# Kernel optimization log

Hardware: AMD Instinct MI355X
Metric: run time of the kernel (lower is better)

The kernel has to match this reference:

```python
import jax, jax.numpy as jnp
import numpy as np

B, N, DIN, H, A = 16384, 32, 275, 64, 14
NEG = 9000000000000000.0  # 9e15, matches torch source


def _att(x, mask, Wv, bv, Wk, bk, Wq, bq):
    # x: [B, N, H], mask: [B, N, N]
    v = jax.nn.relu(x @ Wv + bv)
    q = jax.nn.relu(x @ Wq + bq)
    k = jax.nn.relu(x @ Wk + bk)
    scores = jnp.einsum('bnh,bmh->bnm', q, k)
    att = jax.nn.softmax(scores * mask - NEG * (1.0 - mask), axis=2)
    return jnp.einsum('bnm,bmh->bnh', att, v)


def setup_inputs() -> dict:
    key = jax.random.key(0)
    ks = jax.random.split(key, 16)
    inputs = jax.random.normal(ks[0], (B * N, DIN), dtype=jnp.float32)
    hidden_state = jnp.zeros((B * N, H), dtype=jnp.float32)
    adj = jax.random.randint(ks[1], (B, N, N), 0, 2).astype(jnp.float32)
    eye = jnp.eye(N, dtype=jnp.float32)
    adj = jnp.maximum(adj, eye)  # agents always attend to themselves
    s = 1.0 / np.sqrt(DIN)
    sh = 1.0 / np.sqrt(H)
    p = {
        'W_enc': jax.random.uniform(ks[2], (DIN, H), minval=-s, maxval=s),
        'b_enc': jax.random.uniform(ks[3], (H,), minval=-s, maxval=s),
        'Wv1': jax.random.uniform(ks[4], (H, H), minval=-sh, maxval=sh),
        'bv1': jnp.zeros((H,), jnp.float32),
        'Wk1': jax.random.uniform(ks[5], (H, H), minval=-sh, maxval=sh),
        'bk1': jnp.zeros((H,), jnp.float32),
        'Wq1': jax.random.uniform(ks[6], (H, H), minval=-sh, maxval=sh),
        'bq1': jnp.zeros((H,), jnp.float32),
        'Wv2': jax.random.uniform(ks[7], (H, H), minval=-sh, maxval=sh),
        'bv2': jnp.zeros((H,), jnp.float32),
        'Wk2': jax.random.uniform(ks[8], (H, H), minval=-sh, maxval=sh),
        'bk2': jnp.zeros((H,), jnp.float32),
        'Wq2': jax.random.uniform(ks[9], (H, H), minval=-sh, maxval=sh),
        'bq2': jnp.zeros((H,), jnp.float32),
        'Wqn': jax.random.uniform(ks[10], (H, A), minval=-sh, maxval=sh),
        'bqn': jax.random.uniform(ks[11], (A,), minval=-sh, maxval=sh),
    }
    return dict(inputs=inputs, hidden_state=hidden_state, adj=adj, **p)


def reference(inputs, hidden_state, adj, W_enc, b_enc,
              Wv1, bv1, Wk1, bk1, Wq1, bq1,
              Wv2, bv2, Wk2, bk2, Wq2, bq2,
              Wqn, bqn):
    h1 = jax.nn.relu(inputs @ W_enc + b_enc)          # [B*N, H]
    h1 = h1.reshape(-1, N, H)                          # [B, N, H]
    h2 = _att(h1, adj, Wv1, bv1, Wk1, bk1, Wq1, bq1)   # [B, N, H]
    h3 = _att(h2, adj, Wv2, bv2, Wk2, bk2, Wq2, bq2)   # [B, N, H]
    q = h3 @ Wqn + bqn                                 # [B, N, A]
    return q, hidden_state
```

## Files before the change

### kernel.cpp

```cpp
#include <hip/hip_runtime.h>

#define NB 16384
#define NN 32
#define DK 275
#define HH 64
#define AA 14
#define Q_ELEMS   ((size_t)NB * NN * AA)
#define HID_ELEMS ((size_t)NB * NN * HH)

typedef unsigned short u16;
typedef unsigned int   u32;
typedef __attribute__((ext_vector_type(8))) short s8v;
typedef __attribute__((ext_vector_type(4))) float f4v;

#define MFMA(a,b,c) __builtin_amdgcn_mfma_f32_16x16x32_bf16((a),(b),(c),0,0,0)

__device__ __forceinline__ u16 bf_hi(float x){
    union{float f; u32 u;} v; v.f = x;
    u32 r = v.u + 0x7fffu + ((v.u >> 16) & 1u);
    return (u16)(r >> 16);
}
__device__ __forceinline__ float bf_f(u16 h){
    union{u32 u; float f;} v; v.u = ((u32)h) << 16; return v.f;
}

#define WSE_OFF 0
#define WSE_SZ  (2*4*9*1024)
#define WSL_SZ  (2*4*2*1024)
#define WSQN_OFF (WSE_SZ + 6*WSL_SZ)

__global__ void prepack_w(const float* __restrict__ We,
                          const float* __restrict__ Wv1, const float* __restrict__ Wk1, const float* __restrict__ Wq1,
                          const float* __restrict__ Wv2, const float* __restrict__ Wk2, const float* __restrict__ Wq2,
                          const float* __restrict__ Wqn, char* __restrict__ ws)
{
    int gid  = blockIdx.x * 256 + threadIdx.x;
    int slot = gid >> 6, lane = gid & 63;
    const float* W; int K, OUT, STEPS, MT; size_t base; int rem;
    if (slot < 72) { W = We; K = DK; OUT = 64; STEPS = 9; MT = 4; base = WSE_OFF; rem = slot; }
    else if (slot < 168) {
        int q = slot - 72; int mat = q >> 4; rem = q & 15;
        W = mat==0?Wv1 : mat==1?Wk1 : mat==2?Wq1 : mat==3?Wv2 : mat==4?Wk2 : Wq2;
        K = 64; OUT = 64; STEPS = 2; MT = 4; base = WSE_SZ + (size_t)mat * WSL_SZ;
    } else { W = Wqn; K = 64; OUT = AA; STEPS = 2; MT = 1; base = WSQN_OFF; rem = slot - 168; }
    int o  = 16 * (((rem / STEPS) % MT)) + (lane & 15);
    int part = (rem / STEPS) / MT;
    int s  = rem % STEPS;
    int kb = 32 * s + 8 * (lane >> 4);
    u16 h[8];
#pragma unroll
    for (int e = 0; e < 8; ++e) {
        int k = kb + e;
        float x = (k < K && o < OUT) ? W[(size_t)k * OUT + o] : 0.f;
        u16 hi = bf_hi(x);
        h[e] = (part == 0) ? hi : bf_hi(x - bf_f(hi));
    }
    uint4 d;
    d.x = (u32)h[0] | ((u32)h[1] << 16);
    d.y = (u32)h[2] | ((u32)h[3] << 16);
    d.z = (u32)h[4] | ((u32)h[5] << 16);
    d.w = (u32)h[6] | ((u32)h[7] << 16);
    *(uint4*)(ws + base + (size_t)rem * 1024 + (size_t)lane * 16) = d;
}

#define SM_XAHI 0
#define SM_XALO 10752
#define SM_XBHI 0
#define SM_XBLO 8704
#define SM_QHI  0
#define SM_QLO  4608
#define SM_KHI  9216
#define SM_KLO  13824
#define SM_VT   18432
#define SM_P    23552
#define SM_HHI  26112
#define SM_HLO  30720
#define SM_ADJ  35328
#define SM_TOT  39424

__device__ __forceinline__ f4v relu4(f4v v){
    f4v r; r[0]=fmaxf(v[0],0.f); r[1]=fmaxf(v[1],0.f);
    r[2]=fmaxf(v[2],0.f); r[3]=fmaxf(v[3],0.f); return r;
}
__device__ __forceinline__ void write_hl4(char* hp, char* lp, f4v v){
    u16 h0=bf_hi(v[0]), h1=bf_hi(v[1]), h2=bf_hi(v[2]), h3=bf_hi(v[3]);
    uint2 hw; hw.x = (u32)h0 | ((u32)h1<<16); hw.y = (u32)h2 | ((u32)h3<<16);
    u16 l0=bf_hi(v[0]-bf_f(h0)), l1=bf_hi(v[1]-bf_f(h1));
    u16 l2=bf_hi(v[2]-bf_f(h2)), l3=bf_hi(v[3]-bf_f(h3));
    uint2 lw; lw.x = (u32)l0 | ((u32)l1<<16); lw.y = (u32)l2 | ((u32)l3<<16);
    *(uint2*)hp = hw; *(uint2*)lp = lw;
}
__device__ __forceinline__ void stage4(char* hrow, char* lrow, int k0,
                                       float x0, float x1, float x2, float x3){
    u16 h0=bf_hi(x0), h1=bf_hi(x1), h2=bf_hi(x2), h3=bf_hi(x3);
    uint2 hw; hw.x=(u32)h0|((u32)h1<<16); hw.y=(u32)h2|((u32)h3<<16);
    u16 l0=bf_hi(x0-bf_f(h0)), l1=bf_hi(x1-bf_f(h1));
    u16 l2=bf_hi(x2-bf_f(h2)), l3=bf_hi(x3-bf_f(h3));
    uint2 lw; lw.x=(u32)l0|((u32)l1<<16); lw.y=(u32)l2|((u32)l3<<16);
    *(uint2*)(hrow + 2*k0) = hw; *(uint2*)(lrow + 2*k0) = lw;
}

__global__ __launch_bounds__(256, 4) void dgn_mfma(
    const float* __restrict__ X, const float* __restrict__ adj,
    const char*  __restrict__ ws,
    const float* __restrict__ b_enc,
    const float* __restrict__ bv1, const float* __restrict__ bk1, const float* __restrict__ bq1,
    const float* __restrict__ bv2, const float* __restrict__ bk2, const float* __restrict__ bq2,
    const float* __restrict__ bqn,
    float* __restrict__ Out)
{
    __shared__ __align__(16) char sm[SM_TOT];
    const int b = blockIdx.x, tid = threadIdx.x;
    const int w = tid >> 6, l = tid & 63, lr = l & 15, lg = l >> 4;
    const int ct  = w & 1;
    const int mt0 = w >> 1, mt1 = (w >> 1) + 2;
    const int agent = 16 * ct + lr;
    const char* wsl = ws + (size_t)l * 16;
    const int t8 = tid & 7, ag8 = tid >> 3;
    const float* xrow = X + (size_t)b * NN * DK + (size_t)ag8 * DK;

    {
        char* hrow = sm + SM_XAHI + ag8 * 336;
        char* lrow = sm + SM_XALO + ag8 * 336;
#pragma unroll
        for (int it = 0; it < 5; ++it) {
            int k0 = 4 * t8 + 32 * it;
            stage4(hrow, lrow, k0, xrow[k0], xrow[k0+1], xrow[k0+2], xrow[k0+3]);
        }
        ((float4*)(sm + SM_ADJ))[tid] = ((const float4*)(adj + (size_t)b * NN * NN))[tid];
    }
    __syncthreads();

    f4v ehh0 = *(const f4v*)(b_enc + 16*mt0 + 4*lg);
    f4v ehh1 = *(const f4v*)(b_enc + 16*mt1 + 4*lg);
    f4v ecx0 = {0.f,0.f,0.f,0.f}, ecx1 = {0.f,0.f,0.f,0.f};
    {
        const char* xh = sm + SM_XAHI + agent*336 + 16*lg;
        const char* xl = sm + SM_XALO + agent*336 + 16*lg;
#pragma unroll
        for (int s = 0; s < 5; ++s) {
            s8v bh = *(const s8v*)(xh + 64*s);
            s8v bl = *(const s8v*)(xl + 64*s);
            s8v a0h = *(const s8v*)(wsl + ((0*4 + mt0)*9 + s) * 1024);
            s8v a0l = *(const s8v*)(wsl + ((1*4 + mt0)*9 + s) * 1024);
            s8v a1h = *(const s8v*)(wsl + ((0*4 + mt1)*9 + s) * 1024);
            s8v a1l = *(const s8v*)(wsl + ((1*4 + mt1)*9 + s) * 1024);
            ehh0 = MFMA(a0h, bh, ehh0); ecx0 = MFMA(a0h, bl, ecx0); ecx0 = MFMA(a0l, bh, ecx0);
            ehh1 = MFMA(a1h, bh, ehh1); ecx1 = MFMA(a1h, bl, ecx1); ecx1 = MFMA(a1l, bh, ecx1);
        }
    }
    __syncthreads();

    {
        char* hrow = sm + SM_XBHI + ag8 * 272;
        char* lrow = sm + SM_XBLO + ag8 * 272;
#pragma unroll
        for (int it = 0; it < 4; ++it) {
            int k0 = 4 * t8 + 32 * it;
            float x[4];
#pragma unroll
            for (int j2 = 0; j2 < 4; ++j2) {
                int k = 160 + k0 + j2;
                x[j2] = (k < DK) ? xrow[k] : 0.f;
            }
            stage4(hrow, lrow, k0, x[0], x[1], x[2], x[3]);
        }
    }
    __syncthreads();

    {
        const char* xh = sm + SM_XBHI + agent*272 + 16*lg;
        const char* xl = sm + SM_XBLO + agent*272 + 16*lg;
#pragma unroll
        for (int s = 5; s < 9; ++s) {
            s8v bh = *(const s8v*)(xh + 64*(s-5));
            s8v bl = *(const s8v*)(xl + 64*(s-5));
            s8v a0h = *(const s8v*)(wsl + ((0*4 + mt0)*9 + s) * 1024);
            s8v a0l = *(const s8v*)(wsl + ((1*4 + mt0)*9 + s) * 1024);
            s8v a1h = *(const s8v*)(wsl + ((0*4 + mt1)*9 + s) * 1024);
            s8v a1l = *(const s8v*)(wsl + ((1*4 + mt1)*9 + s) * 1024);
            ehh0 = MFMA(a0h, bh, ehh0); ecx0 = MFMA(a0h, bl, ecx0); ecx0 = MFMA(a0l, bh, ecx0);
            ehh1 = MFMA(a1h, bh, ehh1); ecx1 = MFMA(a1h, bl, ecx1); ecx1 = MFMA(a1l, bh, ecx1);
        }
        write_hl4(sm + SM_HHI + agent*144 + (16*mt0 + 4*lg)*2,
                  sm + SM_HLO + agent*144 + (16*mt0 + 4*lg)*2, relu4(ehh0 + ecx0));
        write_hl4(sm + SM_HHI + agent*144 + (16*mt1 + 4*lg)*2,
                  sm + SM_HLO + agent*144 + (16*mt1 + 4*lg)*2, relu4(ehh1 + ecx1));
    }
    __syncthreads();

#pragma unroll
    for (int layer = 0; layer < 2; ++layer) {
        const float* bv = layer ? bv2 : bv1;
        const float* bk = layer ? bk2 : bk1;
        const float* bq = layer ? bq2 : bq1;
        const size_t lbase = WSE_SZ + (size_t)layer * 3 * WSL_SZ;

        {
            f4v hh[3][2], cx[3][2];
            hh[0][0] = *(const f4v*)(bv + 16*mt0 + 4*lg); hh[0][1] = *(const f4v*)(bv + 16*mt1 + 4*lg);
            hh[1][0] = *(const f4v*)(bk + 16*mt0 + 4*lg); hh[1][1] = *(const f4v*)(bk + 16*mt1 + 4*lg);
            hh[2][0] = *(const f4v*)(bq + 16*mt0 + 4*lg); hh[2][1] = *(const f4v*)(bq + 16*mt1 + 4*lg);
#pragma unroll
            for (int m = 0; m < 3; ++m) { cx[m][0] = f4v{0.f,0.f,0.f,0.f}; cx[m][1] = f4v{0.f,0.f,0.f,0.f}; }
            const char* hH = sm + SM_HHI + agent * 144 + 16*lg;
            const char* hL = sm + SM_HLO + agent * 144 + 16*lg;
#pragma unroll
            for (int s = 0; s < 2; ++s) {
                s8v bh = *(const s8v*)(hH + 64*s);
                s8v bl = *(const s8v*)(hL + 64*s);
#pragma unroll
                for (int m = 0; m < 3; ++m) {
                    const char* wb = wsl + lbase + (size_t)m * WSL_SZ;
                    s8v a0h = *(const s8v*)(wb + ((0*4 + mt0)*2 + s) * 1024);
                    s8v a0l = *(const s8v*)(wb + ((1*4 + mt0)*2 + s) * 1024);
                    s8v a1h = *(const s8v*)(wb + ((0*4 + mt1)*2 + s) * 1024);
                    s8v a1l = *(const s8v*)(wb + ((1*4 + mt1)*2 + s) * 1024);
                    hh[m][0] = MFMA(a0h, bh, hh[m][0]);
                    cx[m][0] = MFMA(a0h, bl, cx[m][0]); cx[m][0] = MFMA(a0l, bh, cx[m][0]);
                    hh[m][1] = MFMA(a1h, bh, hh[m][1]);
                    cx[m][1] = MFMA(a1h, bl, cx[m][1]); cx[m][1] = MFMA(a1l, bh, cx[m][1]);
                }
            }
#pragma unroll
            for (int t = 0; t < 2; ++t) {
                int mt = t ? mt1 : mt0;
                f4v vv = relu4(hh[0][t] + cx[0][t]);
#pragma unroll
                for (int r = 0; r < 4; ++r)
                    *(u16*)(sm + SM_VT + (16*mt + 4*lg + r)*80 + agent*2) = bf_hi(vv[r]);
                write_hl4(sm + SM_KHI + agent*144 + (16*mt + 4*lg)*2,
                          sm + SM_KLO + agent*144 + (16*mt + 4*lg)*2, relu4(hh[1][t] + cx[1][t]));
                write_hl4(sm + SM_QHI + agent*144 + (16*mt + 4*lg)*2,
                          sm + SM_QLO + agent*144 + (16*mt + 4*lg)*2, relu4(hh[2][t] + cx[2][t]));
            }
        }
        __syncthreads();

        if (w < 2) {
            f4v shh[2] = {{0.f,0.f,0.f,0.f},{0.f,0.f,0.f,0.f}};
            f4v scx[2] = {{0.f,0.f,0.f,0.f},{0.f,0.f,0.f,0.f}};
            const char* qH = sm + SM_QHI + (16*w + lr)*144 + 16*lg;
            const char* qL = sm + SM_QLO + (16*w + lr)*144 + 16*lg;
#pragma unroll
            for (int s = 0; s < 2; ++s) {
                s8v ah = *(const s8v*)(qH + 64*s);
                s8v al = *(const s8v*)(qL + 64*s);
#pragma unroll
                for (int t = 0; t < 2; ++t) {
                    s8v bh = *(const s8v*)(sm + SM_KHI + (16*t + lr)*144 + 16*lg + 64*s);
                    s8v bl = *(const s8v*)(sm + SM_KLO + (16*t + lr)*144 + 16*lg + 64*s);
                    shh[t] = MFMA(ah, bh, shh[t]);
                    scx[t] = MFMA(ah, bl, scx[t]); scx[t] = MFMA(al, bh, scx[t]);
                }
            }
            const float* ad = (const float*)(sm + SM_ADJ);
#pragma unroll
            for (int r = 0; r < 4; ++r) {
                int row = 16*w + 4*lg + r;
                float m0 = ad[row*32 + lr], m1 = ad[row*32 + 16 + lr];
                float v0 = (shh[0][r] + scx[0][r]) * m0 - 9e15f * (1.f - m0);
                float v1 = (shh[1][r] + scx[1][r]) * m1 - 9e15f * (1.f - m1);
                float mx = fmaxf(v0, v1);
#pragma unroll
                for (int off = 8; off; off >>= 1) mx = fmaxf(mx, __shfl_xor(mx, off, 16));
                float e0 = __expf(v0 - mx), e1 = __expf(v1 - mx);
                float ssum = e0 + e1;
#pragma unroll
                for (int off = 8; off; off >>= 1) ssum += __shfl_xor(ssum, off, 16);
                float inv = 1.f / ssum;
                *(u16*)(sm + SM_P + row*80 + lr*2)      = bf_hi(e0 * inv);
                *(u16*)(sm + SM_P + row*80 + (16+lr)*2) = bf_hi(e1 * inv);
            }
        }
        __syncthreads();

        {
            s8v pb  = *(const s8v*)(sm + SM_P  + (16*ct  + lr)*80 + 16*lg);
            s8v va0 = *(const s8v*)(sm + SM_VT + (16*mt0 + lr)*80 + 16*lg);
            s8v va1 = *(const s8v*)(sm + SM_VT + (16*mt1 + lr)*80 + 16*lg);
            f4v h0 = {0.f,0.f,0.f,0.f}, h1 = {0.f,0.f,0.f,0.f};
            h0 = MFMA(va0, pb, h0);
            h1 = MFMA(va1, pb, h1);
            write_hl4(sm + SM_HHI + agent*144 + (16*mt0 + 4*lg)*2,
                      sm + SM_HLO + agent*144 + (16*mt0 + 4*lg)*2, h0);
            write_hl4(sm + SM_HHI + agent*144 + (16*mt1 + 4*lg)*2,
                      sm + SM_HLO + agent*144 + (16*mt1 + 4*lg)*2, h1);
        }
        __syncthreads();
    }

    if (w < 2) {
        const int ag = 16 * w + lr;
        f4v hacc, cacc = {0.f,0.f,0.f,0.f};
#pragma unroll
        for (int r = 0; r < 4; ++r) { int a = 4*lg + r; hacc[r] = (a < AA) ? bqn[a] : 0.f; }
        const char* hH = sm + SM_HHI + ag * 144 + 16*lg;
        const char* hL = sm + SM_HLO + ag * 144 + 16*lg;
#pragma unroll
        for (int s = 0; s < 2; ++s) {
            s8v bh = *(const s8v*)(hH + 64*s);
            s8v bl = *(const s8v*)(hL + 64*s);
            s8v ah = *(const s8v*)(wsl + WSQN_OFF + (0*2 + s) * 1024);
            s8v al = *(const s8v*)(wsl + WSQN_OFF + (1*2 + s) * 1024);
            hacc = MFMA(ah, bh, hacc);
            cacc = MFMA(ah, bl, cacc); cacc = MFMA(al, bh, cacc);
        }
        f4v acc = hacc + cacc;
        float* op = Out + ((size_t)b * NN + ag) * AA;
#pragma unroll
        for (int r = 0; r < 4; ++r) { int a = 4*lg + r; if (a < AA) op[a] = acc[r]; }
    }
}

__global__ void copy_hidden(const float4* __restrict__ src,
                            float4* __restrict__ dst, int n4)
{
    int i = blockIdx.x * blockDim.x + threadIdx.x;
    int stride = gridDim.x * blockDim.x;
    for (; i < n4; i += stride) dst[i] = src[i];
}

extern "C" void kernel_launch(void* const* d_in, const int* in_sizes, int n_in,
                              void* d_out, int out_size, void* d_ws, size_t ws_size,
                              hipStream_t stream)
{
    const float* X    = (const float*)d_in[0];
    const float* hid  = (const float*)d_in[1];
    const float* adj  = (const float*)d_in[2];
    const float* W_enc = (const float*)d_in[3];
    const float* b_enc = (const float*)d_in[4];
    const float* Wv1 = (const float*)d_in[5];  const float* bv1 = (const float*)d_in[6];
    const float* Wk1 = (const float*)d_in[7];  const float* bk1 = (const float*)d_in[8];
    const float* Wq1 = (const float*)d_in[9];  const float* bq1 = (const float*)d_in[10];
    const float* Wv2 = (const float*)d_in[11]; const float* bv2 = (const float*)d_in[12];
    const float* Wk2 = (const float*)d_in[13]; const float* bk2 = (const float*)d_in[14];
    const float* Wq2 = (const float*)d_in[15]; const float* bq2 = (const float*)d_in[16];
    const float* Wqn = (const float*)d_in[17]; const float* bqn = (const float*)d_in[18];
    float* out = (float*)d_out;
    char* ws = (char*)d_ws;

    prepack_w<<<43, 256, 0, stream>>>(W_enc, Wv1, Wk1, Wq1, Wv2, Wk2, Wq2, Wqn, ws);

    dgn_mfma<<<NB, 256, 0, stream>>>(X, adj, ws, b_enc,
                                     bv1, bk1, bq1, bv2, bk2, bq2, bqn, out);

    copy_hidden<<<2048, 256, 0, stream>>>((const float4*)hid,
                                          (float4*)(out + Q_ELEMS),
                                          (int)(HID_ELEMS / 4));
}
```

Measured before the change: 398.7 us.

## Load encoder inputs straight into MFMA registers, drop LDS staging and adj buffer

The encoder GEMM now reads each agent's input row directly from global memory into MFMA B-operand registers and does the bf16 hi/lo split in registers. This removes the two LDS staging passes and three block barriers. The adjacency mask is loaded into registers by the two softmax waves instead of being staged in LDS, which shrinks shared memory and may allow more resident blocks. Cross-term accumulators are split into independent chains to shorten MFMA dependency stalls, and bf16 rounding uses the HIP intrinsic. In exchange, global reads are unaligned per lane and less coalesced (each lane reads 32 contiguous bytes from rows with a 275-float stride), and register pressure rises.

Result: slower. 500.2 us (+25.5%).

```diff
diff --git a/kernel.cpp b/kernel.cpp
--- a/kernel.cpp
+++ b/kernel.cpp
@@ -1,4 +1,5 @@
 #include <hip/hip_runtime.h>
+#include <hip/hip_bf16.h>
 
 #define NB 16384
 #define NN 32
@@ -12,13 +13,12 @@
 typedef unsigned int   u32;
 typedef __attribute__((ext_vector_type(8))) short s8v;
 typedef __attribute__((ext_vector_type(4))) float f4v;
+typedef float f4u __attribute__((ext_vector_type(4), aligned(4)));
 
 #define MFMA(a,b,c) __builtin_amdgcn_mfma_f32_16x16x32_bf16((a),(b),(c),0,0,0)
 
 __device__ __forceinline__ u16 bf_hi(float x){
-    union{float f; u32 u;} v; v.f = x;
-    u32 r = v.u + 0x7fffu + ((v.u >> 16) & 1u);
-    return (u16)(r >> 16);
+    return __bfloat16_as_ushort(__float2bfloat16(x));
 }
 __device__ __forceinline__ float bf_f(u16 h){
     union{u32 u; float f;} v; v.u = ((u32)h) << 16; return v.f;
@@ -63,10 +63,6 @@
     *(uint4*)(ws + base + (size_t)rem * 1024 + (size_t)lane * 16) = d;
 }
 
-#define SM_XAHI 0
-#define SM_XALO 10752
-#define SM_XBHI 0
-#define SM_XBLO 8704
 #define SM_QHI  0
 #define SM_QLO  4608
 #define SM_KHI  9216
@@ -75,8 +71,7 @@
 #define SM_P    23552
 #define SM_HHI  26112
 #define SM_HLO  30720
-#define SM_ADJ  35328
-#define SM_TOT  39424
+#define SM_TOT  35328
 
 __device__ __forceinline__ f4v relu4(f4v v){
     f4v r; r[0]=fmaxf(v[0],0.f); r[1]=fmaxf(v[1],0.f);
@@ -89,15 +84,6 @@
     u16 l2=bf_hi(v[2]-bf_f(h2)), l3=bf_hi(v[3]-bf_f(h3));
     uint2 lw; lw.x = (u32)l0 | ((u32)l1<<16); lw.y = (u32)l2 | ((u32)l3<<16);
     *(uint2*)hp = hw; *(uint2*)lp = lw;
-}
-__device__ __forceinline__ void stage4(char* hrow, char* lrow, int k0,
-                                       float x0, float x1, float x2, float x3){
-    u16 h0=bf_hi(x0), h1=bf_hi(x1), h2=bf_hi(x2), h3=bf_hi(x3);
-    uint2 hw; hw.x=(u32)h0|((u32)h1<<16); hw.y=(u32)h2|((u32)h3<<16);
-    u16 l0=bf_hi(x0-bf_f(h0)), l1=bf_hi(x1-bf_f(h1));
-    u16 l2=bf_hi(x2-bf_f(h2)), l3=bf_hi(x3-bf_f(h3));
-    uint2 lw; lw.x=(u32)l0|((u32)l1<<16); lw.y=(u32)l2|((u32)l3<<16);
-    *(uint2*)(hrow + 2*k0) = hw; *(uint2*)(lrow + 2*k0) = lw;
 }
 
 __global__ __launch_bounds__(256, 4) void dgn_mfma(
@@ -116,76 +102,57 @@
     const int mt0 = w >> 1, mt1 = (w >> 1) + 2;
     const int agent = 16 * ct + lr;
     const char* wsl = ws + (size_t)l * 16;
-    const int t8 = tid & 7, ag8 = tid >> 3;
-    const float* xrow = X + (size_t)b * NN * DK + (size_t)ag8 * DK;
+
+    float adjm[4][2];
+    if (w < 2) {
+        const float* ar = adj + (size_t)b * NN * NN;
+#pragma unroll
+        for (int r = 0; r < 4; ++r) {
+            int row = 16*w + 4*lg + r;
+            adjm[r][0] = ar[row * 32 + lr];
+            adjm[r][1] = ar[row * 32 + 16 + lr];
+        }
+    }
 
     {
-        char* hrow = sm + SM_XAHI + ag8 * 336;
-        char* lrow = sm + SM_XALO + ag8 * 336;
-#pragma unroll
-        for (int it = 0; it < 5; ++it) {
-            int k0 = 4 * t8 + 32 * it;
-            stage4(hrow, lrow, k0, xrow[k0], xrow[k0+1], xrow[k0+2], xrow[k0+3]);
-        }
-        ((float4*)(sm + SM_ADJ))[tid] = ((const float4*)(adj + (size_t)b * NN * NN))[tid];
-    }
-    __syncthreads();
-
-    f4v ehh0 = *(const f4v*)(b_enc + 16*mt0 + 4*lg);
-    f4v ehh1 = *(const f4v*)(b_enc + 16*mt1 + 4*lg);
-    f4v ecx0 = {0.f,0.f,0.f,0.f}, ecx1 = {0.f,0.f,0.f,0.f};
-    {
-        const char* xh = sm + SM_XAHI + agent*336 + 16*lg;
-        const char* xl = sm + SM_XALO + agent*336 + 16*lg;
-#pragma unroll
-        for (int s = 0; s < 5; ++s) {
-            s8v bh = *(const s8v*)(xh + 64*s);
-            s8v bl = *(const s8v*)(xl + 64*s);
+        const float* xrow = X + ((size_t)b * NN + agent) * DK;
+        f4v ehh0 = *(const f4v*)(b_enc + 16*mt0 + 4*lg);
+        f4v ehh1 = *(const f4v*)(b_enc + 16*mt1 + 4*lg);
+        f4v ea0 = {0.f,0.f,0.f,0.f}, eb0 = {0.f,0.f,0.f,0.f};
+        f4v ea1 = {0.f,0.f,0.f,0.f}, eb1 = {0.f,0.f,0.f,0.f};
+#pragma unroll
+        for (int s = 0; s < 9; ++s) {
+            float xv[8];
+            if (s < 8) {
+                f4u p0 = *(const f4u*)(xrow + 32*s + 8*lg);
+                f4u p1 = *(const f4u*)(xrow + 32*s + 8*lg + 4);
+#pragma unroll
+                for (int e = 0; e < 4; ++e) { xv[e] = p0[e]; xv[4+e] = p1[e]; }
+            } else {
+#pragma unroll
+                for (int e = 0; e < 8; ++e) {
+                    int k = 256 + 8*lg + e;
+                    xv[e] = (k < DK) ? xrow[k] : 0.f;
+                }
+            }
+            s8v bh, bl;
+#pragma unroll
+            for (int e = 0; e < 8; ++e) {
+                u16 hh = bf_hi(xv[e]);
+                bh[e] = (short)hh;
+                bl[e] = (short)bf_hi(xv[e] - bf_f(hh));
+            }
             s8v a0h = *(const s8v*)(wsl + ((0*4 + mt0)*9 + s) * 1024);
             s8v a0l = *(const s8v*)(wsl + ((1*4 + mt0)*9 + s) * 1024);
             s8v a1h = *(const s8v*)(wsl + ((0*4 + mt1)*9 + s) * 1024);
             s8v a1l = *(const s8v*)(wsl + ((1*4 + mt1)*9 + s) * 1024);
-            ehh0 = MFMA(a0h, bh, ehh0); ecx0 = MFMA(a0h, bl, ecx0); ecx0 = MFMA(a0l, bh, ecx0);
-            ehh1 = MFMA(a1h, bh, ehh1); ecx1 = MFMA(a1h, bl, ecx1); ecx1 = MFMA(a1l, bh, ecx1);
-        }
-    }
-    __syncthreads();
-
-    {
-        char* hrow = sm + SM_XBHI + ag8 * 272;
-        char* lrow = sm + SM_XBLO + ag8 * 272;
-#pragma unroll
-        for (int it = 0; it < 4; ++it) {
-            int k0 = 4 * t8 + 32 * it;
-            float x[4];
-#pragma unroll
-            for (int j2 = 0; j2 < 4; ++j2) {
-                int k = 160 + k0 + j2;
-                x[j2] = (k < DK) ? xrow[k] : 0.f;
-            }
-            stage4(hrow, lrow, k0, x[0], x[1], x[2], x[3]);
-        }
-    }
-    __syncthreads();
-
-    {
-        const char* xh = sm + SM_XBHI + agent*272 + 16*lg;
-        const char* xl = sm + SM_XBLO + agent*272 + 16*lg;
-#pragma unroll
-        for (int s = 5; s < 9; ++s) {
-            s8v bh = *(const s8v*)(xh + 64*(s-5));
-            s8v bl = *(const s8v*)(xl + 64*(s-5));
-            s8v a0h = *(const s8v*)(wsl + ((0*4 + mt0)*9 + s) * 1024);
-            s8v a0l = *(const s8v*)(wsl + ((1*4 + mt0)*9 + s) * 1024);
-            s8v a1h = *(const s8v*)(wsl + ((0*4 + mt1)*9 + s) * 1024);
-            s8v a1l = *(const s8v*)(wsl + ((1*4 + mt1)*9 + s) * 1024);
-            ehh0 = MFMA(a0h, bh, ehh0); ecx0 = MFMA(a0h, bl, ecx0); ecx0 = MFMA(a0l, bh, ecx0);
-            ehh1 = MFMA(a1h, bh, ehh1); ecx1 = MFMA(a1h, bl, ecx1); ecx1 = MFMA(a1l, bh, ecx1);
+            ehh0 = MFMA(a0h, bh, ehh0); ea0 = MFMA(a0h, bl, ea0); eb0 = MFMA(a0l, bh, eb0);
+            ehh1 = MFMA(a1h, bh, ehh1); ea1 = MFMA(a1h, bl, ea1); eb1 = MFMA(a1l, bh, eb1);
         }
         write_hl4(sm + SM_HHI + agent*144 + (16*mt0 + 4*lg)*2,
-                  sm + SM_HLO + agent*144 + (16*mt0 + 4*lg)*2, relu4(ehh0 + ecx0));
+                  sm + SM_HLO + agent*144 + (16*mt0 + 4*lg)*2, relu4(ehh0 + ea0 + eb0));
         write_hl4(sm + SM_HHI + agent*144 + (16*mt1 + 4*lg)*2,
-                  sm + SM_HLO + agent*144 + (16*mt1 + 4*lg)*2, relu4(ehh1 + ecx1));
+                  sm + SM_HLO + agent*144 + (16*mt1 + 4*lg)*2, relu4(ehh1 + ea1 + eb1));
     }
     __syncthreads();
 
@@ -239,7 +206,8 @@
 
         if (w < 2) {
             f4v shh[2] = {{0.f,0.f,0.f,0.f},{0.f,0.f,0.f,0.f}};
-            f4v scx[2] = {{0.f,0.f,0.f,0.f},{0.f,0.f,0.f,0.f}};
+            f4v sca[2] = {{0.f,0.f,0.f,0.f},{0.f,0.f,0.f,0.f}};
+            f4v scb[2] = {{0.f,0.f,0.f,0.f},{0.f,0.f,0.f,0.f}};
             const char* qH = sm + SM_QHI + (16*w + lr)*144 + 16*lg;
             const char* qL = sm + SM_QLO + (16*w + lr)*144 + 16*lg;
 #pragma unroll
@@ -251,16 +219,16 @@
                     s8v bh = *(const s8v*)(sm + SM_KHI + (16*t + lr)*144 + 16*lg + 64*s);
                     s8v bl = *(const s8v*)(sm + SM_KLO + (16*t + lr)*144 + 16*lg + 64*s);
                     shh[t] = MFMA(ah, bh, shh[t]);
-                    scx[t] = MFMA(ah, bl, scx[t]); scx[t] = MFMA(al, bh, scx[t]);
+                    sca[t] = MFMA(ah, bl, sca[t]);
+                    scb[t] = MFMA(al, bh, scb[t]);
                 }
             }
-            const float* ad = (const float*)(sm + SM_ADJ);
 #pragma unroll
             for (int r = 0; r < 4; ++r) {
                 int row = 16*w + 4*lg + r;
-                float m0 = ad[row*32 + lr], m1 = ad[row*32 + 16 + lr];
-                float v0 = (shh[0][r] + scx[0][r]) * m0 - 9e15f * (1.f - m0);
-                float v1 = (shh[1][r] + scx[1][r]) * m1 - 9e15f * (1.f - m1);
+                float m0 = adjm[r][0], m1 = adjm[r][1];
+                float v0 = (shh[0][r] + sca[0][r] + scb[0][r]) * m0 - 9e15f * (1.f - m0);
+                float v1 = (shh[1][r] + sca[1][r] + scb[1][r]) * m1 - 9e15f * (1.f - m1);
                 float mx = fmaxf(v0, v1);
 #pragma unroll
                 for (int off = 8; off; off >>= 1) mx = fmaxf(mx, __shfl_xor(mx, off, 16));
```
